# Optimization experiments

Measured on AMD Instinct MI355X. Metric: run time of the kernel, lower is better.

## Reference

```python
import jax, jax.numpy as jnp
import numpy as np
from jax import lax

N, C, H, W = 4, 256, 64, 64
R = 2          # upsample ratio (scale_factor)
K = 5          # CARAFE up_kernel
COMP = 64      # CARAFEPack compressed_channels
EPS = 1e-5     # BatchNorm eps


def setup_inputs() -> dict:
    key = jax.random.key(0)
    ks = jax.random.split(key, 8)
    w = lambda k, s: jax.random.normal(k, s, jnp.float32) * 0.05
    return {
        "low_feature": jax.random.normal(ks[0], (N, C, H * R, W * R), jnp.float32),
        "high_feature": jax.random.normal(ks[1], (N, C, H, W), jnp.float32),
        "w_cc": w(ks[2], (COMP, C, 1, 1)),            # channel compressor 1x1
        "b_cc": jnp.zeros((COMP,), jnp.float32),
        "w_ce": w(ks[3], (K * K * R * R, COMP, 3, 3)), # content encoder 3x3
        "b_ce": jnp.zeros((K * K * R * R,), jnp.float32),
        "w_conv2": w(ks[4], (C, C, 1, 1)),
        "b_conv2": jnp.zeros((C,), jnp.float32),
        "w_bott": w(ks[5], (C, 2 * C, 1, 1)),          # bottleneck 1x1, no bias
        "gamma": jnp.ones((C,), jnp.float32),
        "beta": jnp.zeros((C,), jnp.float32),
    }


def _conv1x1(x, w, b=None):
    y = jnp.einsum('nchw,oc->nohw', x, w[:, :, 0, 0])
    if b is not None:
        y = y + b[None, :, None, None]
    return y


def _conv3x3(x, w, b):
    y = lax.conv_general_dilated(x, w, (1, 1), [(1, 1), (1, 1)],
                                 dimension_numbers=('NCHW', 'OIHW', 'NCHW'))
    return y + b[None, :, None, None]


def _pixel_shuffle(x, r):
    n, c, h, w = x.shape
    c2 = c // (r * r)
    x = x.reshape(n, c2, r, r, h, w).transpose(0, 1, 4, 2, 5, 3)
    return x.reshape(n, c2, h * r, w * r)


def _carafe(x, w_cc, b_cc, w_ce, b_ce):
    n, c, h, w = x.shape
    # predicted kernels: compress -> encode -> pixel_shuffle -> softmax over k^2
    mask = _conv3x3(_conv1x1(x, w_cc, b_cc), w_ce, b_ce)      # [N, K*K*R*R, H, W]
    mask = _pixel_shuffle(mask, R)                            # [N, K*K, H*R, W*R]
    mask = jax.nn.softmax(mask, axis=1)                       # group=1 -> over K*K
    # k x k neighborhoods of x (zero-padded), kernel index = ky*K + kx
    pad = K // 2
    xp = jnp.pad(x, ((0, 0), (0, 0), (pad, pad), (pad, pad)))
    patches = jnp.stack([xp[:, :, dy:dy + h, dx:dx + w]
                         for dy in range(K) for dx in range(K)], axis=2)  # [N,C,K*K,H,W]
    # each output pixel (i,j) reads source (i//R, j//R) neighborhood
    mr = mask.reshape(n, K * K, h, R, w, R)
    out = jnp.einsum('nckhw,nkhawb->nchawb', patches, mr)
    return out.reshape(n, c, h * R, w * R)


def reference(low_feature, high_feature, w_cc, b_cc, w_ce, b_ce,
              w_conv2, b_conv2, w_bott, gamma, beta):
    hf = _carafe(high_feature, w_cc, b_cc, w_ce, b_ce)        # [N,C,H*R,W*R]
    value = _conv1x1(hf, w_conv2, b_conv2)
    x = jnp.concatenate([value, hf], axis=1)                  # [N,2C,.,.]
    x = _conv1x1(x, w_bott)
    # BatchNorm (training-mode batch statistics) + ReLU
    mean = jnp.mean(x, axis=(0, 2, 3), keepdims=True)
    var = jnp.var(x, axis=(0, 2, 3), keepdims=True)
    x = (x - mean) * lax.rsqrt(var + EPS)
    x = x * gamma[None, :, None, None] + beta[None, :, None, None]
    return jax.nn.relu(x)
```

## Files before the change

### kernel.cpp

```cpp
#include <hip/hip_runtime.h>
#include <hip/hip_bf16.h>

#define N_    4
#define C_    256
#define PS_   4096
#define PO_   16384
#define COMP_ 64
#define QCH_  100

typedef unsigned short u16;
typedef __attribute__((ext_vector_type(8))) short short8;
typedef __attribute__((ext_vector_type(4))) float f32x4;

__device__ __forceinline__ u16 f2bu(float f) {
    __hip_bfloat16 h = __float2bfloat16(f);
    return __builtin_bit_cast(u16, h);
}
__device__ __forceinline__ float bits2f(unsigned u) {
    union { unsigned i; float f; } v; v.i = u; return v.f;
}

__global__ __launch_bounds__(256) void k_prep(const float* __restrict__ w_bott,
        const float* __restrict__ w_conv2, const float* __restrict__ b_conv2,
        const float* __restrict__ w_ce, const float* __restrict__ w_cc,
        u16* __restrict__ Weff_bf, float* __restrict__ beff,
        u16* __restrict__ Wb, u16* __restrict__ Wcc_bf) {
    int bid = blockIdx.x;
    if (bid < 256) {
        int o = bid, c = threadIdx.x;
        __shared__ float wb[512];
        wb[c]       = w_bott[o * 512 + c];
        wb[c + 256] = w_bott[o * 512 + 256 + c];
        __syncthreads();
        float acc = wb[256 + c];
        #pragma unroll 8
        for (int m = 0; m < 256; ++m)
            acc += wb[m] * w_conv2[m * 256 + c];
        Weff_bf[o * 256 + c] = f2bu(acc);
        if (c == 0) {
            float be = 0.f;
            for (int m = 0; m < 256; ++m) be += wb[m] * b_conv2[m];
            beff[o] = be;
        }
    } else if (bid < 544) {
        int i = (bid - 256) * 256 + threadIdx.x;
        int q = i / 576, u = i - q * 576;
        float v = (q < 100) ? w_ce[q * 576 + u] : 0.f;
        Wb[i] = f2bu(v);
    } else {
        int j = (bid - 544) * 256 + threadIdx.x;
        Wcc_bf[j] = f2bu(w_cc[j]);
    }
}

__global__ __launch_bounds__(256) void k_compress_mfma(const u16* __restrict__ Wcc_bf,
        const float* __restrict__ high, const float* __restrict__ b_cc,
        float* __restrict__ comp) {
    int tid = threadIdx.x;
    int wid = tid >> 6, lane = tid & 63;
    int col = lane & 15, quad = lane >> 4;
    int px0 = blockIdx.x * 64;
    int n = px0 >> 12, pxb = px0 & 4095;
    __shared__ u16 As[64 * 40];
    __shared__ u16 Bs[64 * 40];
    f32x4 acc[4] = {};
    #pragma unroll 1
    for (int k0 = 0; k0 < 256; k0 += 32) {
        __syncthreads();
        {
            int row = tid >> 2, seg = tid & 3;
            short8 av = *reinterpret_cast<const short8*>(Wcc_bf + row * 256 + k0 + seg * 8);
            *reinterpret_cast<short8*>(&As[row * 40 + seg * 8]) = av;
        }
        #pragma unroll
        for (int it = 0; it < 4; ++it) {
            int idx = it * 256 + tid;
            int c = (idx >> 6) * 2, px = idx & 63;
            const float* hp = high + (n * C_ + k0 + c) * PS_ + pxb + px;
            unsigned lo = f2bu(hp[0]);
            unsigned hi = f2bu(hp[PS_]);
            *reinterpret_cast<unsigned*>(&Bs[px * 40 + c]) = lo | (hi << 16);
        }
        __syncthreads();
        short8 a = *reinterpret_cast<const short8*>(&As[(wid * 16 + col) * 40 + quad * 8]);
        #pragma unroll
        for (int nt = 0; nt < 4; ++nt) {
            short8 b = *reinterpret_cast<const short8*>(&Bs[(nt * 16 + col) * 40 + quad * 8]);
            acc[nt] = __builtin_amdgcn_mfma_f32_16x16x32_bf16(a, b, acc[nt], 0, 0, 0);
        }
    }
    #pragma unroll
    for (int r = 0; r < 4; ++r) {
        int m = wid * 16 + quad * 4 + r;
        float bias = b_cc[m];
        float* cp = comp + (n * COMP_ + m) * PS_ + pxb + col;
        #pragma unroll
        for (int nt = 0; nt < 4; ++nt)
            cp[nt * 16] = acc[nt][r] + bias;
    }
}

__global__ __launch_bounds__(256) void k_im2col(const float* __restrict__ comp,
        u16* __restrict__ Icol) {
    int b = blockIdx.x;
    int n = b >> 6, tile = b & 63;
    int ty0 = (tile >> 3) << 3, tx0 = (tile & 7) << 3;
    int tid = threadIdx.x;
    __shared__ float ct[64 * 100];
    for (int idx = tid; idx < 6400; idx += 256) {
        int cc = idx / 100, r = idx - cc * 100;
        int yy = ty0 - 1 + r / 10, xx = tx0 - 1 + (r % 10);
        float v = 0.f;
        if ((unsigned)yy < 64u && (unsigned)xx < 64u)
            v = comp[(n * COMP_ + cc) * PS_ + yy * 64 + xx];
        ct[idx] = v;
    }
    __syncthreads();
    int u0 = tid * 2, u1 = u0 + 1;
    int c0 = (unsigned)u0 / 9u, t0 = u0 - c0 * 9;
    int c1 = (unsigned)u1 / 9u, t1 = u1 - c1 * 9;
    int off0 = c0 * 100 + (t0 / 3) * 10 + (t0 % 3);
    int off1 = c1 * 100 + (t1 / 3) * 10 + (t1 % 3);
    int u2 = 512 + tid * 2, u3 = u2 + 1;
    int c2 = (unsigned)u2 / 9u, t2 = u2 - c2 * 9;
    int c3 = (unsigned)u3 / 9u, t3 = u3 - c3 * 9;
    int off2 = c2 * 100 + (t2 / 3) * 10 + (t2 % 3);
    int off3 = c3 * 100 + (t3 / 3) * 10 + (t3 % 3);
    #pragma unroll 1
    for (int px = 0; px < 64; ++px) {
        int py = px >> 3, pxx = px & 7;
        int base = py * 10 + pxx;
        int gpx = n * PS_ + (ty0 + py) * 64 + tx0 + pxx;
        u16* dst = Icol + gpx * 576;
        unsigned lo = f2bu(ct[off0 + base]);
        unsigned hi = f2bu(ct[off1 + base]);
        *reinterpret_cast<unsigned*>(dst + u0) = lo | (hi << 16);
        if (tid < 32) {
            unsigned lo2 = f2bu(ct[off2 + base]);
            unsigned hi2 = f2bu(ct[off3 + base]);
            *reinterpret_cast<unsigned*>(dst + u2) = lo2 | (hi2 << 16);
        }
    }
}

__global__ __launch_bounds__(256) void k_encode_mfma(const u16* __restrict__ Wb,
        const u16* __restrict__ Icol, const float* __restrict__ b_ce,
        float* __restrict__ mask_raw) {
    int tid = threadIdx.x;
    int wid = tid >> 6, lane = tid & 63;
    int col = lane & 15, quad = lane >> 4;
    int px0 = blockIdx.x * 64;
    int n = px0 >> 12, pxb = px0 & 4095;
    __shared__ u16 As[128 * 40];
    __shared__ u16 Bs[64 * 40];
    f32x4 acc[2][4] = {};
    #pragma unroll 1
    for (int k0 = 0; k0 < 576; k0 += 32) {
        __syncthreads();
        #pragma unroll
        for (int it = 0; it < 2; ++it) {
            int s = tid + it * 256;
            int row = s >> 2, seg = s & 3;
            short8 av = *reinterpret_cast<const short8*>(Wb + row * 576 + k0 + seg * 8);
            *reinterpret_cast<short8*>(&As[row * 40 + seg * 8]) = av;
        }
        {
            int row = tid >> 2, seg = tid & 3;
            short8 bv = *reinterpret_cast<const short8*>(Icol + (px0 + row) * 576 + k0 + seg * 8);
            *reinterpret_cast<short8*>(&Bs[row * 40 + seg * 8]) = bv;
        }
        __syncthreads();
        short8 a0 = *reinterpret_cast<const short8*>(&As[(wid * 32 + col) * 40 + quad * 8]);
        short8 a1 = *reinterpret_cast<const short8*>(&As[(wid * 32 + 16 + col) * 40 + quad * 8]);
        #pragma unroll
        for (int nt = 0; nt < 4; ++nt) {
            short8 b = *reinterpret_cast<const short8*>(&Bs[(nt * 16 + col) * 40 + quad * 8]);
            acc[0][nt] = __builtin_amdgcn_mfma_f32_16x16x32_bf16(a0, b, acc[0][nt], 0, 0, 0);
            acc[1][nt] = __builtin_amdgcn_mfma_f32_16x16x32_bf16(a1, b, acc[1][nt], 0, 0, 0);
        }
    }
    #pragma unroll
    for (int mi = 0; mi < 2; ++mi) {
        int qbase = (wid * 2 + mi) * 16 + quad * 4;
        #pragma unroll
        for (int r = 0; r < 4; ++r) {
            int q = qbase + r;
            if (q < 100) {
                float bias = b_ce[q];
                float* mp = mask_raw + (n * QCH_ + q) * PS_ + pxb + col;
                #pragma unroll
                for (int nt = 0; nt < 4; ++nt)
                    mp[nt * 16] = acc[mi][nt][r] + bias;
            }
        }
    }
}

__global__ __launch_bounds__(256) void k_ygemm_mfma(const u16* __restrict__ Weff_bf,
        const float* __restrict__ high, u16* __restrict__ Yt) {
    int tid = threadIdx.x;
    int wid = tid >> 6, lane = tid & 63;
    int col = lane & 15, quad = lane >> 4;
    int px0 = blockIdx.x * 128;
    int o0 = blockIdx.y * 128;
    int n = px0 >> 12, pxb = px0 & 4095;
    __shared__ u16 As[128 * 40];
    __shared__ u16 Bs[128 * 40];
    f32x4 acc[2][8] = {};
    #pragma unroll 1
    for (int k0 = 0; k0 < 256; k0 += 32) {
        __syncthreads();
        #pragma unroll
        for (int it = 0; it < 2; ++it) {
            int s = tid + it * 256;
            int row = s >> 2, seg = s & 3;
            short8 av = *reinterpret_cast<const short8*>(Weff_bf + (o0 + row) * 256 + k0 + seg * 8);
            *reinterpret_cast<short8*>(&As[row * 40 + seg * 8]) = av;
        }
        #pragma unroll
        for (int it = 0; it < 8; ++it) {
            int idx = it * 256 + tid;
            int c = (idx >> 7) * 2, px = idx & 127;
            const float* hp = high + (n * C_ + k0 + c) * PS_ + pxb + px;
            unsigned lo = f2bu(hp[0]);
            unsigned hi = f2bu(hp[PS_]);
            *reinterpret_cast<unsigned*>(&Bs[px * 40 + c]) = lo | (hi << 16);
        }
        __syncthreads();
        short8 a0 = *reinterpret_cast<const short8*>(&As[(wid * 32 + col) * 40 + quad * 8]);
        short8 a1 = *reinterpret_cast<const short8*>(&As[(wid * 32 + 16 + col) * 40 + quad * 8]);
        #pragma unroll
        for (int nt = 0; nt < 8; ++nt) {
            short8 b = *reinterpret_cast<const short8*>(&Bs[(nt * 16 + col) * 40 + quad * 8]);
            acc[0][nt] = __builtin_amdgcn_mfma_f32_16x16x32_bf16(a0, b, acc[0][nt], 0, 0, 0);
            acc[1][nt] = __builtin_amdgcn_mfma_f32_16x16x32_bf16(a1, b, acc[1][nt], 0, 0, 0);
        }
    }
    #pragma unroll
    for (int mi = 0; mi < 2; ++mi) {
        int ob = o0 + wid * 32 + mi * 16 + quad * 4;
        #pragma unroll
        for (int nt = 0; nt < 8; ++nt) {
            int gpx = px0 + nt * 16 + col;
            unsigned lo = f2bu(acc[mi][nt][0]) | ((unsigned)f2bu(acc[mi][nt][1]) << 16);
            unsigned hi = f2bu(acc[mi][nt][2]) | ((unsigned)f2bu(acc[mi][nt][3]) << 16);
            uint2 pk; pk.x = lo; pk.y = hi;
            *reinterpret_cast<uint2*>(Yt + (size_t)gpx * 256 + ob) = pk;
        }
    }
}

__global__ __launch_bounds__(256) void k_carafe(const u16* __restrict__ Yt,
        const float* __restrict__ mask_raw, const float* __restrict__ beff,
        float* __restrict__ xout) {
    int tile = blockIdx.x, n = blockIdx.y, half = blockIdx.z;
    int sh0 = (tile >> 3) << 3, sw0 = (tile & 7) << 3;
    int tid = threadIdx.x;
    int px = tid & 63, g = tid >> 6;
    int ly = px >> 3, lx = px & 7;
    int h = sh0 + ly, w = sw0 + lx;

    __shared__ float mt[6400];
    __shared__ u16 xt[144 * 68];

    for (int idx = tid; idx < 6400; idx += 256) {
        int q = idx >> 6, p = idx & 63;
        mt[idx] = mask_raw[(n * QCH_ + q) * PS_ + (sh0 + (p >> 3)) * 64 + sw0 + (p & 7)];
    }
    __syncthreads();

    float vs[4][25];
    #pragma unroll
    for (int s = 0; s < 4; ++s) {
        #pragma unroll
        for (int k = 0; k < 25; ++k) vs[s][k] = mt[(k * 4 + s) * 64 + px];
        float mx = vs[s][0];
        #pragma unroll
        for (int k = 1; k < 25; ++k) mx = fmaxf(mx, vs[s][k]);
        float sum = 0.f;
        #pragma unroll
        for (int k = 0; k < 25; ++k) { vs[s][k] = __expf(vs[s][k] - mx); sum += vs[s][k]; }
        float inv = 1.f / sum;
        #pragma unroll
        for (int k = 0; k < 25; ++k) vs[s][k] *= inv;
    }

    const u16* Yb = Yt + (size_t)n * PS_ * 256;
    float* hp_base = xout + (size_t)(n * C_) * PO_;
    #pragma unroll 1
    for (int chunk = 0; chunk < 2; ++chunk) {
        int ch0 = half * 128 + chunk * 64;
        __syncthreads();
        for (int idx = tid; idx < 1152; idx += 256) {
            int sp = idx >> 3, seg = idx & 7;
            int row = sp / 12, colm = sp - row * 12;
            int yy = sh0 - 2 + row, xx = sw0 - 2 + colm;
            short8 val = {};
            if ((unsigned)yy < 64u && (unsigned)xx < 64u)
                val = *reinterpret_cast<const short8*>(Yb + (size_t)(yy * 64 + xx) * 256 + ch0 + seg * 8);
            *reinterpret_cast<short8*>(&xt[sp * 68 + seg * 8]) = val;
        }
        __syncthreads();
        #pragma unroll 1
        for (int cq = 0; cq < 4; ++cq) {
            int c = g * 16 + cq * 4;
            int ch = ch0 + c;
            f32x4 bv = *reinterpret_cast<const f32x4*>(beff + ch);
            float a_[4][4];
            #pragma unroll
            for (int s = 0; s < 4; ++s) {
                a_[s][0] = bv[0]; a_[s][1] = bv[1]; a_[s][2] = bv[2]; a_[s][3] = bv[3];
            }
            const u16* bp = xt + (ly * 12 + lx) * 68 + c;
            #pragma unroll
            for (int ky = 0; ky < 5; ++ky) {
                #pragma unroll
                for (int kx = 0; kx < 5; ++kx) {
                    uint2 rv = *reinterpret_cast<const uint2*>(bp + (ky * 12 + kx) * 68);
                    float f0 = bits2f(rv.x << 16);
                    float f1 = bits2f(rv.x & 0xffff0000u);
                    float f2 = bits2f(rv.y << 16);
                    float f3 = bits2f(rv.y & 0xffff0000u);
                    int k = ky * 5 + kx;
                    #pragma unroll
                    for (int s = 0; s < 4; ++s) {
                        float m = vs[s][k];
                        a_[s][0] += m * f0; a_[s][1] += m * f1;
                        a_[s][2] += m * f2; a_[s][3] += m * f3;
                    }
                }
            }
            #pragma unroll
            for (int i = 0; i < 4; ++i) {
                float* op = hp_base + (size_t)(ch + i) * PO_ + (2 * h) * 128 + 2 * w;
                float2 r0; r0.x = a_[0][i]; r0.y = a_[1][i];
                float2 r1; r1.x = a_[2][i]; r1.y = a_[3][i];
                *reinterpret_cast<float2*>(op) = r0;
                *reinterpret_cast<float2*>(op + 128) = r1;
            }
        }
    }
}

__global__ __launch_bounds__(256) void k_stats(const float* __restrict__ xb,
        const float* __restrict__ gamma, const float* __restrict__ beta,
        float* __restrict__ scale, float* __restrict__ shift) {
    int o = blockIdx.x, tid = threadIdx.x;
    float s = 0.f, s2 = 0.f;
    for (int n = 0; n < 4; ++n) {
        const float* p = xb + (size_t)(n * C_ + o) * PO_;
        #pragma unroll 4
        for (int i = 0; i < 64; ++i) {
            float v = p[i * 256 + tid];
            s += v; s2 += v * v;
        }
    }
    __shared__ float rs[256], rq[256];
    rs[tid] = s; rq[tid] = s2;
    __syncthreads();
    for (int off = 128; off > 0; off >>= 1) {
        if (tid < off) { rs[tid] += rs[tid + off]; rq[tid] += rq[tid + off]; }
        __syncthreads();
    }
    if (tid == 0) {
        float mean = rs[0] * (1.f / 65536.f);
        float var  = rq[0] * (1.f / 65536.f) - mean * mean;
        float sc = rsqrtf(var + 1e-5f) * gamma[o];
        scale[o] = sc;
        shift[o] = beta[o] - mean * sc;
    }
}

__global__ __launch_bounds__(256) void k_norm(float* __restrict__ xb,
        const float* __restrict__ scale, const float* __restrict__ shift) {
    int base = (blockIdx.x * 256 + threadIdx.x) * 4;
    int o = (base >> 14) & 255;
    float sc = scale[o], sh = shift[o];
    float4 v = *reinterpret_cast<const float4*>(xb + base);
    v.x = fmaxf(v.x * sc + sh, 0.f);
    v.y = fmaxf(v.y * sc + sh, 0.f);
    v.z = fmaxf(v.z * sc + sh, 0.f);
    v.w = fmaxf(v.w * sc + sh, 0.f);
    *reinterpret_cast<float4*>(xb + base) = v;
}

extern "C" void kernel_launch(void* const* d_in, const int* in_sizes, int n_in,
                              void* d_out, int out_size, void* d_ws, size_t ws_size,
                              hipStream_t stream) {
    const float* high    = (const float*)d_in[1];
    const float* w_cc    = (const float*)d_in[2];
    const float* b_cc    = (const float*)d_in[3];
    const float* w_ce    = (const float*)d_in[4];
    const float* b_ce    = (const float*)d_in[5];
    const float* w_conv2 = (const float*)d_in[6];
    const float* b_conv2 = (const float*)d_in[7];
    const float* w_bott  = (const float*)d_in[8];
    const float* gamma   = (const float*)d_in[9];
    const float* beta    = (const float*)d_in[10];

    char* ws = (char*)d_ws;
    float* beff    = (float*)(ws + 0);
    float* scale   = (float*)(ws + 1024);
    float* shift   = (float*)(ws + 2048);
    u16*   Weff_bf = (u16*)  (ws + 3072);
    u16*   Wcc_bf  = (u16*)  (ws + 134144);
    u16*   Wb      = (u16*)  (ws + 166912);
    float* mask    = (float*)(ws + 314368);
    float* comp    = (float*)(ws + 314368);
    u16*   Icol    = (u16*)  (ws + 6867968);
    u16*   Yt      = (u16*)  (ws + 6867968);
    float* xout    = (float*)d_out;

    k_prep         <<<608, 256, 0, stream>>>(w_bott, w_conv2, b_conv2, w_ce, w_cc,
                                             Weff_bf, beff, Wb, Wcc_bf);
    k_compress_mfma<<<256, 256, 0, stream>>>(Wcc_bf, high, b_cc, comp);
    k_im2col       <<<256, 256, 0, stream>>>(comp, Icol);
    k_encode_mfma  <<<256, 256, 0, stream>>>(Wb, Icol, b_ce, mask);
    k_ygemm_mfma   <<<dim3(128, 2), 256, 0, stream>>>(Weff_bf, high, Yt);
    k_carafe       <<<dim3(64, 4, 2), 256, 0, stream>>>(Yt, mask, beff, xout);
    k_stats        <<<256, 256, 0, stream>>>(xout, gamma, beta, scale, shift);
    k_norm         <<<16384, 256, 0, stream>>>(xout, scale, shift);
}
```

Before: 270.7 us.

## Fuse BatchNorm partial statistics into CARAFE kernel and restructure its work split

The CARAFE kernel now computes per-channel partial sums and sums of squares with wavefront shuffles and writes them to a small workspace, so k_stats only reduces 512 partials per channel instead of rereading the full 64 MB output. The grid is also split four ways over channels, each block handles one 64-channel chunk, and each wave covers two of the four subpixels with 32 channels. This lowers registers per thread and allows more blocks per CU. Softmax mask values are loaded straight from global memory into registers rather than staged in shared memory. The costs are redundant mask and softmax work across the channel blocks, plus extra shuffle reductions and partial-sum stores.

Result: slower. 294.9 us (+9.0%).

```diff
diff --git a/kernel.cpp b/kernel.cpp
--- a/kernel.cpp
+++ b/kernel.cpp
@@ -250,113 +250,114 @@
     }
 }
 
-__global__ __launch_bounds__(256) void k_carafe(const u16* __restrict__ Yt,
+__global__ __launch_bounds__(256, 4) void k_carafe(const u16* __restrict__ Yt,
         const float* __restrict__ mask_raw, const float* __restrict__ beff,
-        float* __restrict__ xout) {
-    int tile = blockIdx.x, n = blockIdx.y, half = blockIdx.z;
+        float* __restrict__ xout, float* __restrict__ ps, float* __restrict__ pq) {
+    int tile = blockIdx.x, n = blockIdx.y, zq = blockIdx.z;
     int sh0 = (tile >> 3) << 3, sw0 = (tile & 7) << 3;
     int tid = threadIdx.x;
     int px = tid & 63, g = tid >> 6;
     int ly = px >> 3, lx = px & 7;
     int h = sh0 + ly, w = sw0 + lx;
-
-    __shared__ float mt[6400];
+    int sp = (g & 1) << 1;
+    int cg = (g >> 1) << 5;
+    int ch0 = zq << 6;
+
     __shared__ u16 xt[144 * 68];
 
-    for (int idx = tid; idx < 6400; idx += 256) {
-        int q = idx >> 6, p = idx & 63;
-        mt[idx] = mask_raw[(n * QCH_ + q) * PS_ + (sh0 + (p >> 3)) * 64 + sw0 + (p & 7)];
+    const u16* Yb = Yt + (size_t)n * PS_ * 256;
+    for (int idx = tid; idx < 1152; idx += 256) {
+        int spix = idx >> 3, seg = idx & 7;
+        int row = spix / 12, colm = spix - row * 12;
+        int yy = sh0 - 2 + row, xx = sw0 - 2 + colm;
+        short8 val = {};
+        if ((unsigned)yy < 64u && (unsigned)xx < 64u)
+            val = *reinterpret_cast<const short8*>(Yb + (size_t)(yy * 64 + xx) * 256 + ch0 + seg * 8);
+        *reinterpret_cast<short8*>(&xt[spix * 68 + seg * 8]) = val;
+    }
+
+    float vs[2][25];
+    {
+        const float* mb = mask_raw + ((size_t)n * QCH_ + sp) * PS_ + h * 64 + w;
+        #pragma unroll
+        for (int j = 0; j < 2; ++j) {
+            #pragma unroll
+            for (int k = 0; k < 25; ++k)
+                vs[j][k] = mb[(size_t)(k * 4 + j) * PS_];
+            float mx = vs[j][0];
+            #pragma unroll
+            for (int k = 1; k < 25; ++k) mx = fmaxf(mx, vs[j][k]);
+            float sum = 0.f;
+            #pragma unroll
+            for (int k = 0; k < 25; ++k) { vs[j][k] = __expf(vs[j][k] - mx); sum += vs[j][k]; }
+            float inv = 1.f / sum;
+            #pragma unroll
+            for (int k = 0; k < 25; ++k) vs[j][k] *= inv;
+        }
     }
     __syncthreads();
 
-    float vs[4][25];
-    #pragma unroll
-    for (int s = 0; s < 4; ++s) {
-        #pragma unroll
-        for (int k = 0; k < 25; ++k) vs[s][k] = mt[(k * 4 + s) * 64 + px];
-        float mx = vs[s][0];
-        #pragma unroll
-        for (int k = 1; k < 25; ++k) mx = fmaxf(mx, vs[s][k]);
-        float sum = 0.f;
-        #pragma unroll
-        for (int k = 0; k < 25; ++k) { vs[s][k] = __expf(vs[s][k] - mx); sum += vs[s][k]; }
-        float inv = 1.f / sum;
-        #pragma unroll
-        for (int k = 0; k < 25; ++k) vs[s][k] *= inv;
-    }
-
-    const u16* Yb = Yt + (size_t)n * PS_ * 256;
-    float* hp_base = xout + (size_t)(n * C_) * PO_;
+    const u16* bp = xt + (ly * 12 + lx) * 68;
+    int row_off = (2 * h + (sp >> 1)) * 128 + 2 * w;
+    int slot = (n * 64 + tile) * 2 + (g & 1);
+    float* hp_base = xout + (size_t)n * C_ * PO_;
+
     #pragma unroll 1
-    for (int chunk = 0; chunk < 2; ++chunk) {
-        int ch0 = half * 128 + chunk * 64;
-        __syncthreads();
-        for (int idx = tid; idx < 1152; idx += 256) {
-            int sp = idx >> 3, seg = idx & 7;
-            int row = sp / 12, colm = sp - row * 12;
-            int yy = sh0 - 2 + row, xx = sw0 - 2 + colm;
-            short8 val = {};
-            if ((unsigned)yy < 64u && (unsigned)xx < 64u)
-                val = *reinterpret_cast<const short8*>(Yb + (size_t)(yy * 64 + xx) * 256 + ch0 + seg * 8);
-            *reinterpret_cast<short8*>(&xt[sp * 68 + seg * 8]) = val;
-        }
-        __syncthreads();
-        #pragma unroll 1
-        for (int cq = 0; cq < 4; ++cq) {
-            int c = g * 16 + cq * 4;
-            int ch = ch0 + c;
-            f32x4 bv = *reinterpret_cast<const f32x4*>(beff + ch);
-            float a_[4][4];
-            #pragma unroll
-            for (int s = 0; s < 4; ++s) {
-                a_[s][0] = bv[0]; a_[s][1] = bv[1]; a_[s][2] = bv[2]; a_[s][3] = bv[3];
+    for (int cq = 0; cq < 8; ++cq) {
+        int c = cg + cq * 4;
+        int ch = ch0 + c;
+        f32x4 bv = *reinterpret_cast<const f32x4*>(beff + ch);
+        float a0[4] = {bv[0], bv[1], bv[2], bv[3]};
+        float a1[4] = {bv[0], bv[1], bv[2], bv[3]};
+        const u16* tp = bp + c;
+        #pragma unroll
+        for (int ky = 0; ky < 5; ++ky) {
+            #pragma unroll
+            for (int kx = 0; kx < 5; ++kx) {
+                uint2 rv = *reinterpret_cast<const uint2*>(tp + (ky * 12 + kx) * 68);
+                float f0 = bits2f(rv.x << 16);
+                float f1 = bits2f(rv.x & 0xffff0000u);
+                float f2 = bits2f(rv.y << 16);
+                float f3 = bits2f(rv.y & 0xffff0000u);
+                int k = ky * 5 + kx;
+                float m0 = vs[0][k], m1 = vs[1][k];
+                a0[0] += m0 * f0; a0[1] += m0 * f1;
+                a0[2] += m0 * f2; a0[3] += m0 * f3;
+                a1[0] += m1 * f0; a1[1] += m1 * f1;
+                a1[2] += m1 * f2; a1[3] += m1 * f3;
             }
-            const u16* bp = xt + (ly * 12 + lx) * 68 + c;
-            #pragma unroll
-            for (int ky = 0; ky < 5; ++ky) {
-                #pragma unroll
-                for (int kx = 0; kx < 5; ++kx) {
-                    uint2 rv = *reinterpret_cast<const uint2*>(bp + (ky * 12 + kx) * 68);
-                    float f0 = bits2f(rv.x << 16);
-                    float f1 = bits2f(rv.x & 0xffff0000u);
-                    float f2 = bits2f(rv.y << 16);
-                    float f3 = bits2f(rv.y & 0xffff0000u);
-                    int k = ky * 5 + kx;
-                    #pragma unroll
-                    for (int s = 0; s < 4; ++s) {
-                        float m = vs[s][k];
-                        a_[s][0] += m * f0; a_[s][1] += m * f1;
-                        a_[s][2] += m * f2; a_[s][3] += m * f3;
-                    }
-                }
+        }
+        #pragma unroll
+        for (int i = 0; i < 4; ++i) {
+            float2 r; r.x = a0[i]; r.y = a1[i];
+            *reinterpret_cast<float2*>(hp_base + (size_t)(ch + i) * PO_ + row_off) = r;
+        }
+        #pragma unroll
+        for (int i = 0; i < 4; ++i) {
+            float s  = a0[i] + a1[i];
+            float q2 = a0[i] * a0[i] + a1[i] * a1[i];
+            #pragma unroll
+            for (int off = 1; off < 64; off <<= 1) {
+                s  += __shfl_xor(s, off);
+                q2 += __shfl_xor(q2, off);
             }
-            #pragma unroll
-            for (int i = 0; i < 4; ++i) {
-                float* op = hp_base + (size_t)(ch + i) * PO_ + (2 * h) * 128 + 2 * w;
-                float2 r0; r0.x = a_[0][i]; r0.y = a_[1][i];
-                float2 r1; r1.x = a_[2][i]; r1.y = a_[3][i];
-                *reinterpret_cast<float2*>(op) = r0;
-                *reinterpret_cast<float2*>(op + 128) = r1;
+            if (px == 0) {
+                ps[(ch + i) * 512 + slot] = s;
+                pq[(ch + i) * 512 + slot] = q2;
             }
         }
     }
 }
 
-__global__ __launch_bounds__(256) void k_stats(const float* __restrict__ xb,
-        const float* __restrict__ gamma, const float* __restrict__ beta,
-        float* __restrict__ scale, float* __restrict__ shift) {
+__global__ __launch_bounds__(256) void k_stats(const float* __restrict__ ps,
+        const float* __restrict__ pq, const float* __restrict__ gamma,
+        const float* __restrict__ beta, float* __restrict__ scale,
+        float* __restrict__ shift) {
     int o = blockIdx.x, tid = threadIdx.x;
-    float s = 0.f, s2 = 0.f;
-    for (int n = 0; n < 4; ++n) {
-        const float* p = xb + (size_t)(n * C_ + o) * PO_;
-        #pragma unroll 4
-        for (int i = 0; i < 64; ++i) {
-            float v = p[i * 256 + tid];
-            s += v; s2 += v * v;
-        }
-    }
+    float s = ps[o * 512 + tid] + ps[o * 512 + 256 + tid];
+    float q = pq[o * 512 + tid] + pq[o * 512 + 256 + tid];
     __shared__ float rs[256], rq[256];
-    rs[tid] = s; rq[tid] = s2;
+    rs[tid] = s; rq[tid] = q;
     __syncthreads();
     for (int off = 128; off > 0; off >>= 1) {
         if (tid < off) { rs[tid] += rs[tid + off]; rq[tid] += rq[tid + off]; }
@@ -409,6 +410,8 @@
     float* comp    = (float*)(ws + 314368);
     u16*   Icol    = (u16*)  (ws + 6867968);
     u16*   Yt      = (u16*)  (ws + 6867968);
+    float* ps      = (float*)(ws + 15256576);
+    float* pq      = (float*)(ws + 15780864);
     float* xout    = (float*)d_out;
 
     k_prep         <<<608, 256, 0, stream>>>(w_bott, w_conv2, b_conv2, w_ce, w_cc,
@@ -417,7 +420,7 @@
     k_im2col       <<<256, 256, 0, stream>>>(comp, Icol);
     k_encode_mfma  <<<256, 256, 0, stream>>>(Wb, Icol, b_ce, mask);
     k_ygemm_mfma   <<<dim3(128, 2), 256, 0, stream>>>(Weff_bf, high, Yt);
-    k_carafe       <<<dim3(64, 4, 2), 256, 0, stream>>>(Yt, mask, beff, xout);
-    k_stats        <<<256, 256, 0, stream>>>(xout, gamma, beta, scale, shift);
+    k_carafe       <<<dim3(64, 4, 4), 256, 0, stream>>>(Yt, mask, beff, xout, ps, pq);
+    k_stats        <<<256, 256, 0, stream>>>(ps, pq, gamma, beta, scale, shift);
     k_norm         <<<16384, 256, 0, stream>>>(xout, scale, shift);
 }
```
